# Optimization experiments

Hardware: AMD Instinct MI355X
Metric: run time of the kernel (lower is better)

The kernel has to match this reference:

```python
import jax, jax.numpy as jnp
import numpy as np

CLIP_MIN = 0.0
CLIP_MAX = 1.0
B, T, F, E, CD = 64, 48, 128, 64, 32


def setup_inputs() -> dict:
    key = jax.random.key(0)
    ks = jax.random.split(key, 8)
    return {
        "input_x": jax.random.uniform(ks[0], (B, T, F), dtype=jnp.float32),
        "mask": jax.random.randint(ks[1], (B, T, F), 0, 2, dtype=jnp.int32),
        "embed0": jax.random.normal(ks[2], (F, E), dtype=jnp.float32) * 0.1,
        "embed1": jax.random.normal(ks[3], (F, E), dtype=jnp.float32) * 0.1,
        "embed_missing": jax.random.normal(ks[4], (F, E), dtype=jnp.float32) * 0.1,
        "attention_f_w": jax.random.normal(ks[5], (F, E), dtype=jnp.float32) * 0.1,
        "attention_f_b": jnp.zeros((F,), dtype=jnp.float32),
        "compress_w": jax.random.normal(ks[6], (2 * E, CD), dtype=jnp.float32) * 0.1,
    }


def reference(input_x, mask, embed0, embed1, embed_missing, attention_f_w, attention_f_b, compress_w):
    b, t, f = input_x.shape
    # new_mask: feature observed anywhere in time -> [b, 1, f, 1] (broadcasts over time)
    m = (jnp.sum(mask, axis=-2) != 0).astype(input_x.dtype)[:, None, :, None]
    x = input_x[..., None]  # [b, t, f, 1]
    # interval embedding c: [b, t, f, e]
    c0 = (x - m * CLIP_MIN) * embed0
    c1 = (m * CLIP_MAX - x) * embed1
    c = (c0 + c1) / (CLIP_MAX - CLIP_MIN) + (1.0 - m) * embed_missing
    # pairwise scores: sum_e c_i * c_j * w_i + b_i  (avoids [b,t,f,f,e] materialization)
    scores = jnp.einsum("btie,btje->btij", c * attention_f_w, c) + attention_f_b[:, None]
    scores = jnp.clip(scores, -5.0, 5.0)
    off_diag = 1.0 - jnp.eye(f, dtype=c.dtype)
    masked_exps = jnp.exp(scores) * off_diag
    attn = masked_exps / (jnp.sum(masked_exps, axis=-1, keepdims=True) + 1e-8)  # [b,t,f,f]
    # weighted aggregation: sum_j attn_ij * (c_i * c_j) = c_i * (attn @ c)_i
    agg = c * jnp.einsum("btij,btje->btie", attn, c)
    a = jax.nn.relu(jnp.concatenate([c, agg], axis=-1))  # [b,t,f,2e]
    out = jnp.einsum("btfk,kd->btfd", a, compress_w)
    return out.reshape(b, t, f * compress_w.shape[-1])
```

## Files before the change

### kernel.cpp

```cpp
#include <hip/hip_runtime.h>

#define NB 64
#define NT 48
#define NF 128
#define NE 64
#define NCD 32

#define LOG2E 1.4426950408889634f
#define SCLO -7.213475204444817f
#define SCHI  7.213475204444817f

typedef __attribute__((ext_vector_type(8))) short bf16x8;
typedef __attribute__((ext_vector_type(4))) float f32x4;
typedef __attribute__((ext_vector_type(2))) uint u32x2;

#define WS_MFLAG 0
#define WS_DB    32768
#define WS_E1B   49152
#define WS_EMB   65536
#define WS_WLB   81920
#define WS_WT    98304
#define WS_BL    106496

__device__ __forceinline__ ushort f2bf(float x) {
    union { float f; uint u; } v; v.f = x;
    uint r = v.u + 0x7fffu + ((v.u >> 16) & 1u);
    return (ushort)(r >> 16);
}
__device__ __forceinline__ uint pk_bf16(float lo, float hi) {
    uint r; asm("v_cvt_pk_bf16_f32 %0, %1, %2" : "=v"(r) : "v"(lo), "v"(hi)); return r;
}
__device__ __forceinline__ float bflo(uint u) { union { uint u; float f; } v; v.u = u << 16; return v.f; }
__device__ __forceinline__ float bfhi(uint u) { union { uint u; float f; } v; v.u = u & 0xffff0000u; return v.f; }

#define TRR(dst, addr, IMM) \
    asm volatile("ds_read_b64_tr_b16 %0, %1 offset:" IMM : "=v"(dst) : "v"(addr))

#define PLSWAP(a, b) asm("v_permlane32_swap_b32 %0, %1" : "+v"(a), "+v"(b))

__global__ __launch_bounds__(256) void prep_kernel(
    const int* __restrict__ mask, const float* __restrict__ e0, const float* __restrict__ e1,
    const float* __restrict__ em, const float* __restrict__ aw, const float* __restrict__ ab,
    const float* __restrict__ cw,
    uint* __restrict__ mflag, ushort* __restrict__ db, ushort* __restrict__ e1b,
    ushort* __restrict__ emb, ushort* __restrict__ wlb, ushort* __restrict__ wt,
    float* __restrict__ bl)
{
    const int blk = blockIdx.x, tid = threadIdx.x;
    if (blk < 32) {
        int idx = blk * 256 + tid;
        float e1v = e1[idx];
        e1b[idx] = f2bf(e1v);
        emb[idx] = f2bf(em[idx]);
        db[idx]  = f2bf(e0[idx] - e1v);
        wlb[idx] = f2bf(aw[idx] * LOG2E);
    } else if (blk < 64) {
        int idx = (blk - 32) * 256 + tid;
        int b = idx >> 7, f = idx & 127;
        const int* p = mask + b * (NT * NF) + f;
        int s = 0;
#pragma unroll
        for (int t = 0; t < NT; ++t) s += p[t * NF];
        mflag[idx] = (s != 0) ? 1u : 0u;
    } else if (blk < 80) {
        int idx = (blk - 64) * 256 + tid;
        int k = idx >> 5, d = idx & 31;
        int kd;
        if (k < 64) kd = k;
        else {
            int kk = k - 64;
            kd = 64 + ((kk & 51) | ((kk & 4) << 1) | ((kk & 8) >> 1));
        }
        wt[d * 128 + kd] = f2bf(cw[idx]);
    } else {
        if (tid < NF) bl[tid] = ab[tid] * LOG2E;
    }
}

__global__ __launch_bounds__(512, 4) void fused_kernel(
    const float* __restrict__ input_x, const uint* __restrict__ mflag,
    const ushort* __restrict__ db, const ushort* __restrict__ e1b, const ushort* __restrict__ emb,
    const ushort* __restrict__ wlb, const float* __restrict__ blog,
    const ushort* __restrict__ wt, float* __restrict__ out)
{
    __shared__ ushort sC[2 * 9248];

    const int tid = threadIdx.x;
    const int blk = blockIdx.x;
    const int b   = blk / 24;
    const int bt0 = b * NT + (blk % 24) * 2;
    const int bt1 = bt0 + 1;

    const int wv = tid >> 6, ln = tid & 63;
    const int lr = ln & 15, lg = ln >> 4;
    const int i0 = wv << 4, irow = i0 + lr;

    const float bl = blog[irow];
    const float x0 = input_x[bt0 * NF + irow];
    const float x1 = input_x[bt1 * NF + irow];
    const ushort* Mrow = (mflag[b * NF + irow] ? e1b : emb) + irow * NE;
    const ushort* Drow = db + irow * NE;
    const ushort* Wrow = wlb + irow * NE;

    const int sbase = (lg >> 1) * 2312 + (lr >> 2) * 72 + (lr & 3) * 16 + (lg & 1) * 8;

    ushort* sC0 = sC;
    ushort* sC1 = sC + 9248;

    bf16x8 cwf0[2], cwf1[2];
#pragma unroll
    for (int ks = 0; ks < 2; ++ks) {
        const int eo = ks * 32 + lg * 8;
        uint d4[4], m4[4], w4[4];
        *(uint4*)d4 = *(const uint4*)(Drow + eo);
        *(uint4*)m4 = *(const uint4*)(Mrow + eo);
        *(uint4*)w4 = *(const uint4*)(Wrow + eo);
        uint cb0[4], cb1[4];
        union { uint u[4]; bf16x8 v; } cw0, cw1;
#pragma unroll
        for (int j = 0; j < 4; ++j) {
            float dlo = bflo(d4[j]), dhi = bfhi(d4[j]);
            float mlo = bflo(m4[j]), mhi = bfhi(m4[j]);
            float wlo = bflo(w4[j]), whi = bfhi(w4[j]);
            float c0lo = fmaf(x0, dlo, mlo), c0hi = fmaf(x0, dhi, mhi);
            float c1lo = fmaf(x1, dlo, mlo), c1hi = fmaf(x1, dhi, mhi);
            cb0[j] = pk_bf16(c0lo, c0hi);
            cb1[j] = pk_bf16(c1lo, c1hi);
            cw0.u[j] = pk_bf16(c0lo * wlo, c0hi * whi);
            cw1.u[j] = pk_bf16(c1lo * wlo, c1hi * whi);
        }
        cwf0[ks] = cw0.v; cwf1[ks] = cw1.v;
        *(uint4*)&sC0[sbase + wv * 288 + ks * 4624] = *(uint4*)cb0;
        *(uint4*)&sC1[sbase + wv * 288 + ks * 4624] = *(uint4*)cb1;
    }
    __syncthreads();

    auto run_S = [&](const ushort* base, bf16x8 w0, bf16x8 w1, f32x4* st) {
#pragma unroll
        for (int jt = 0; jt < 8; ++jt) {
            f32x4 a = (f32x4){bl, bl, bl, bl};
            bf16x8 a0 = *(bf16x8*)&base[sbase + jt * 288];
            a = __builtin_amdgcn_mfma_f32_16x16x32_bf16(a0, w0, a, 0, 0, 0);
            bf16x8 a1 = *(bf16x8*)&base[sbase + jt * 288 + 4624];
            a = __builtin_amdgcn_mfma_f32_16x16x32_bf16(a1, w1, a, 0, 0, 0);
            st[jt] = a;
        }
    };
    auto run_SM = [&](f32x4* st, uint* pp) -> float {
        float rs0 = 0.f, rs1 = 0.f, rs2 = 0.f, rs3 = 0.f;
#pragma unroll
        for (int jt = 0; jt < 8; ++jt) {
            f32x4 v = st[jt];
            float e0 = exp2f(__builtin_amdgcn_fmed3f(v[0], SCLO, SCHI));
            float e1 = exp2f(__builtin_amdgcn_fmed3f(v[1], SCLO, SCHI));
            float e2 = exp2f(__builtin_amdgcn_fmed3f(v[2], SCLO, SCHI));
            float e3 = exp2f(__builtin_amdgcn_fmed3f(v[3], SCLO, SCHI));
            if (jt == wv) {
                const bool on = (lg == (lr >> 2));
                e0 = (on && (lr & 3) == 0) ? 0.f : e0;
                e1 = (on && (lr & 3) == 1) ? 0.f : e1;
                e2 = (on && (lr & 3) == 2) ? 0.f : e2;
                e3 = (on && (lr & 3) == 3) ? 0.f : e3;
            }
            rs0 += e0; rs1 += e1; rs2 += e2; rs3 += e3;
            pp[2 * jt]     = pk_bf16(e0, e1);
            pp[2 * jt + 1] = pk_bf16(e2, e3);
        }
        float rs = (rs0 + rs1) + (rs2 + rs3);
        rs += __shfl_xor(rs, 16);
        rs += __shfl_xor(rs, 32);
        return 1.0f / (rs + 1e-8f);
    };
    auto run_AGG = [&](const ushort* base, uint* pp, f32x4* ag) {
#pragma unroll
        for (int et = 0; et < 4; ++et) ag[et] = (f32x4){0.f, 0.f, 0.f, 0.f};
        const uint tb0 = (uint)(uintptr_t)base
                       + 2u * (uint)(72 * (((lg >> 1) << 2) + (lg & 1)) + lr);
#pragma unroll
        for (int ks = 0; ks < 4; ++ks) {
            uint X0 = pp[4 * ks], X1 = pp[4 * ks + 1], X2 = pp[4 * ks + 2], X3 = pp[4 * ks + 3];
            PLSWAP(X0, X2);
            PLSWAP(X1, X3);
            union { uint u[4]; bf16x8 v; } pf;
            pf.u[0] = X0; pf.u[1] = X1; pf.u[2] = X2; pf.u[3] = X3;
            const uint tb = tb0 + 1152u * (uint)ks;
            u32x2 c0a, c0b, c1a, c1b, c2a, c2b, c3a, c3b;
            TRR(c0a, tb, "0");     TRR(c0b, tb, "144");
            TRR(c1a, tb, "4624");  TRR(c1b, tb, "4768");
            TRR(c2a, tb, "9248");  TRR(c2b, tb, "9392");
            TRR(c3a, tb, "13872"); TRR(c3b, tb, "14016");
            asm volatile("s_waitcnt lgkmcnt(0)" ::: "memory");
            __builtin_amdgcn_sched_barrier(0);
            union { u32x2 d[2]; bf16x8 v; } a0, a1, a2, a3;
            a0.d[0] = c0a; a0.d[1] = c0b;
            a1.d[0] = c1a; a1.d[1] = c1b;
            a2.d[0] = c2a; a2.d[1] = c2b;
            a3.d[0] = c3a; a3.d[1] = c3b;
            ag[0] = __builtin_amdgcn_mfma_f32_16x16x32_bf16(a0.v, pf.v, ag[0], 0, 0, 0);
            ag[1] = __builtin_amdgcn_mfma_f32_16x16x32_bf16(a1.v, pf.v, ag[1], 0, 0, 0);
            ag[2] = __builtin_amdgcn_mfma_f32_16x16x32_bf16(a2.v, pf.v, ag[2], 0, 0, 0);
            ag[3] = __builtin_amdgcn_mfma_f32_16x16x32_bf16(a3.v, pf.v, ag[3], 0, 0, 0);
        }
    };
    auto run_EPI = [&](const ushort* base, f32x4* ag, float inv, uint* aa) {
        const int ebase = (wv * 4 + (lr >> 2)) * 72 + (lr & 3) * 16 + lg * 4;
#pragma unroll
        for (int et = 0; et < 4; ++et) {
            u32x2 cb2 = *(u32x2*)&base[ebase + et * 2312];
            float a0f = fmaxf(ag[et][0] * inv * bflo(cb2.x), 0.f);
            float a1f = fmaxf(ag[et][1] * inv * bfhi(cb2.x), 0.f);
            float a2f = fmaxf(ag[et][2] * inv * bflo(cb2.y), 0.f);
            float a3f = fmaxf(ag[et][3] * inv * bfhi(cb2.y), 0.f);
            aa[2 * et]     = pk_bf16(a0f, a1f);
            aa[2 * et + 1] = pk_bf16(a2f, a3f);
        }
    };
    auto run_OUT = [&](const ushort* base, uint* aa, const bf16x8* wf, int bt) {
        f32x4 oc[2];
        oc[0] = (f32x4){0.f, 0.f, 0.f, 0.f};
        oc[1] = (f32x4){0.f, 0.f, 0.f, 0.f};
#pragma unroll
        for (int ks = 0; ks < 4; ++ks) {
            bf16x8 afr;
            if (ks < 2) {
                const uint4 cc = *(uint4*)&base[sbase + wv * 288 + ks * 4624];
                union { uint u[4]; bf16x8 v; } rl;
                asm("v_pk_max_i16 %0, %1, 0" : "=v"(rl.u[0]) : "v"(cc.x));
                asm("v_pk_max_i16 %0, %1, 0" : "=v"(rl.u[1]) : "v"(cc.y));
                asm("v_pk_max_i16 %0, %1, 0" : "=v"(rl.u[2]) : "v"(cc.z));
                asm("v_pk_max_i16 %0, %1, 0" : "=v"(rl.u[3]) : "v"(cc.w));
                afr = rl.v;
            } else {
                const int kk = ks - 2;
                uint Y0 = aa[4 * kk], Y1 = aa[4 * kk + 1], Y2 = aa[4 * kk + 2], Y3 = aa[4 * kk + 3];
                PLSWAP(Y0, Y2);
                PLSWAP(Y1, Y3);
                union { uint u[4]; bf16x8 v; } af;
                af.u[0] = Y0; af.u[1] = Y1; af.u[2] = Y2; af.u[3] = Y3;
                afr = af.v;
            }
            oc[0] = __builtin_amdgcn_mfma_f32_16x16x32_bf16(afr, wf[ks * 2 + 0], oc[0], 0, 0, 0);
            oc[1] = __builtin_amdgcn_mfma_f32_16x16x32_bf16(afr, wf[ks * 2 + 1], oc[1], 0, 0, 0);
        }
        float* op = out + bt * (NF * NCD);
#pragma unroll
        for (int dt = 0; dt < 2; ++dt)
#pragma unroll
            for (int r = 0; r < 4; ++r)
                op[(i0 + lg * 4 + r) * NCD + dt * 16 + lr] = oc[dt][r];
    };

    f32x4 st0[8], st1[8];
    uint pp0[16], pp1[16];
    f32x4 ag0[4], ag1[4];
    uint aa0[8], aa1[8];

    run_S(sC0, cwf0[0], cwf0[1], st0);
    const float inv0 = run_SM(st0, pp0);
    run_S(sC1, cwf1[0], cwf1[1], st1);
    const float inv1 = run_SM(st1, pp1);

    run_AGG(sC0, pp0, ag0);
    run_EPI(sC0, ag0, inv0, aa0);
    run_AGG(sC1, pp1, ag1);

    bf16x8 wf[8];
#pragma unroll
    for (int ks = 0; ks < 4; ++ks)
#pragma unroll
        for (int dt = 0; dt < 2; ++dt)
            wf[ks * 2 + dt] = *(const bf16x8*)(wt + (dt * 16 + lr) * 128 + ks * 32 + lg * 8);

    run_EPI(sC1, ag1, inv1, aa1);
    run_OUT(sC0, aa0, wf, bt0);
    run_OUT(sC1, aa1, wf, bt1);
}

extern "C" void kernel_launch(void* const* d_in, const int* in_sizes, int n_in,
                              void* d_out, int out_size, void* d_ws, size_t ws_size,
                              hipStream_t stream) {
    const float* input_x       = (const float*)d_in[0];
    const int*   mask          = (const int*)d_in[1];
    const float* embed0        = (const float*)d_in[2];
    const float* embed1        = (const float*)d_in[3];
    const float* embed_missing = (const float*)d_in[4];
    const float* attn_w        = (const float*)d_in[5];
    const float* attn_b        = (const float*)d_in[6];
    const float* compress_w    = (const float*)d_in[7];
    float* out = (float*)d_out;

    char* ws = (char*)d_ws;
    uint*   mflag = (uint*)(ws + WS_MFLAG);
    ushort* dbp   = (ushort*)(ws + WS_DB);
    ushort* e1bp  = (ushort*)(ws + WS_E1B);
    ushort* embp  = (ushort*)(ws + WS_EMB);
    ushort* wlbp  = (ushort*)(ws + WS_WLB);
    ushort* wtp   = (ushort*)(ws + WS_WT);
    float*  blp   = (float*)(ws + WS_BL);

    hipLaunchKernelGGL(prep_kernel, dim3(81), dim3(256), 0, stream,
                       mask, embed0, embed1, embed_missing, attn_w, attn_b, compress_w,
                       mflag, dbp, e1bp, embp, wlbp, wtp, blp);
    hipLaunchKernelGGL(fused_kernel, dim3(NB * NT / 2), dim3(512), 0, stream,
                       input_x, mflag, dbp, e1bp, embp, wlbp, blp, wtp, out);
}
```

Before: 43.11 us.

## Halve waves per block, each wave processes two 16-row tiles sharing transposed C loads

The fused kernel now launches 4 waves of 256 threads instead of 8, and each wave handles 32 feature rows as two 16-row groups. In the aggregation step the transposed LDS reads of C are shared between both groups' MFMAs, and the compress stage issues two accumulator sets per wave. This aims to halve redundant LDS traffic per block and increase MFMA work per wave, at the cost of more registers per wave and fewer waves to hide latency.

After: 56.35 us. 1.31x slower.

```diff
diff --git a/kernel.cpp b/kernel.cpp
--- a/kernel.cpp
+++ b/kernel.cpp
@@ -35,7 +35,6 @@
 
 #define TRR(dst, addr, IMM) \
     asm volatile("ds_read_b64_tr_b16 %0, %1 offset:" IMM : "=v"(dst) : "v"(addr))
-
 #define PLSWAP(a, b) asm("v_permlane32_swap_b32 %0, %1" : "+v"(a), "+v"(b))
 
 __global__ __launch_bounds__(256) void prep_kernel(
@@ -77,7 +76,7 @@
     }
 }
 
-__global__ __launch_bounds__(512, 4) void fused_kernel(
+__global__ __launch_bounds__(256, 4) void fused_kernel(
     const float* __restrict__ input_x, const uint* __restrict__ mflag,
     const ushort* __restrict__ db, const ushort* __restrict__ e1b, const ushort* __restrict__ emb,
     const ushort* __restrict__ wlb, const float* __restrict__ blog,
@@ -93,60 +92,67 @@
 
     const int wv = tid >> 6, ln = tid & 63;
     const int lr = ln & 15, lg = ln >> 4;
-    const int i0 = wv << 4, irow = i0 + lr;
-
-    const float bl = blog[irow];
-    const float x0 = input_x[bt0 * NF + irow];
-    const float x1 = input_x[bt1 * NF + irow];
-    const ushort* Mrow = (mflag[b * NF + irow] ? e1b : emb) + irow * NE;
-    const ushort* Drow = db + irow * NE;
-    const ushort* Wrow = wlb + irow * NE;
-
-    const int sbase = (lg >> 1) * 2312 + (lr >> 2) * 72 + (lr & 3) * 16 + (lg & 1) * 8;
+    const int irow0 = wv * 32 + lr;
 
     ushort* sC0 = sC;
     ushort* sC1 = sC + 9248;
 
-    bf16x8 cwf0[2], cwf1[2];
-#pragma unroll
-    for (int ks = 0; ks < 2; ++ks) {
-        const int eo = ks * 32 + lg * 8;
-        uint d4[4], m4[4], w4[4];
-        *(uint4*)d4 = *(const uint4*)(Drow + eo);
-        *(uint4*)m4 = *(const uint4*)(Mrow + eo);
-        *(uint4*)w4 = *(const uint4*)(Wrow + eo);
-        uint cb0[4], cb1[4];
-        union { uint u[4]; bf16x8 v; } cw0, cw1;
-#pragma unroll
-        for (int j = 0; j < 4; ++j) {
-            float dlo = bflo(d4[j]), dhi = bfhi(d4[j]);
-            float mlo = bflo(m4[j]), mhi = bfhi(m4[j]);
-            float wlo = bflo(w4[j]), whi = bfhi(w4[j]);
-            float c0lo = fmaf(x0, dlo, mlo), c0hi = fmaf(x0, dhi, mhi);
-            float c1lo = fmaf(x1, dlo, mlo), c1hi = fmaf(x1, dhi, mhi);
-            cb0[j] = pk_bf16(c0lo, c0hi);
-            cb1[j] = pk_bf16(c1lo, c1hi);
-            cw0.u[j] = pk_bf16(c0lo * wlo, c0hi * whi);
-            cw1.u[j] = pk_bf16(c1lo * wlo, c1hi * whi);
-        }
-        cwf0[ks] = cw0.v; cwf1[ks] = cw1.v;
-        *(uint4*)&sC0[sbase + wv * 288 + ks * 4624] = *(uint4*)cb0;
-        *(uint4*)&sC1[sbase + wv * 288 + ks * 4624] = *(uint4*)cb1;
+    const int abase = (lg >> 1) * 2312 + (lr >> 2) * 72 + (lr & 3) * 16 + (lg & 1) * 8;
+
+    const float bl0 = blog[irow0];
+    const float bl1 = blog[irow0 + 16];
+
+    bf16x8 cwf0[2][2], cwf1[2][2];
+#pragma unroll
+    for (int g = 0; g < 2; ++g) {
+        const int irow = irow0 + g * 16;
+        const float xa = input_x[bt0 * NF + irow];
+        const float xb = input_x[bt1 * NF + irow];
+        const ushort* Mrow = (mflag[b * NF + irow] ? e1b : emb) + irow * NE;
+        const ushort* Drow = db + irow * NE;
+        const ushort* Wrow = wlb + irow * NE;
+#pragma unroll
+        for (int ks = 0; ks < 2; ++ks) {
+            const int eo = ks * 32 + lg * 8;
+            uint d4[4], m4[4], w4[4];
+            *(uint4*)d4 = *(const uint4*)(Drow + eo);
+            *(uint4*)m4 = *(const uint4*)(Mrow + eo);
+            *(uint4*)w4 = *(const uint4*)(Wrow + eo);
+            uint cb0[4], cb1[4];
+            union { uint u[4]; bf16x8 v; } ca, cb;
+#pragma unroll
+            for (int j = 0; j < 4; ++j) {
+                float dlo = bflo(d4[j]), dhi = bfhi(d4[j]);
+                float mlo = bflo(m4[j]), mhi = bfhi(m4[j]);
+                float wlo = bflo(w4[j]), whi = bfhi(w4[j]);
+                float c0lo = fmaf(xa, dlo, mlo), c0hi = fmaf(xa, dhi, mhi);
+                float c1lo = fmaf(xb, dlo, mlo), c1hi = fmaf(xb, dhi, mhi);
+                cb0[j] = pk_bf16(c0lo, c0hi);
+                cb1[j] = pk_bf16(c1lo, c1hi);
+                ca.u[j] = pk_bf16(c0lo * wlo, c0hi * whi);
+                cb.u[j] = pk_bf16(c1lo * wlo, c1hi * whi);
+            }
+            cwf0[g][ks] = ca.v; cwf1[g][ks] = cb.v;
+            const int so = abase + (wv * 2 + g) * 288 + ks * 4624;
+            *(uint4*)&sC0[so] = *(uint4*)cb0;
+            *(uint4*)&sC1[so] = *(uint4*)cb1;
+        }
     }
     __syncthreads();
 
-    auto run_S = [&](const ushort* base, bf16x8 w0, bf16x8 w1, f32x4* st) {
+    auto run_S = [&](const ushort* base, bf16x8 w0, bf16x8 w1, float blv, f32x4* st) {
 #pragma unroll
         for (int jt = 0; jt < 8; ++jt) {
-            f32x4 a = (f32x4){bl, bl, bl, bl};
-            bf16x8 a0 = *(bf16x8*)&base[sbase + jt * 288];
+            f32x4 a = (f32x4){blv, blv, blv, blv};
+            bf16x8 a0 = *(bf16x8*)&base[abase + jt * 288];
             a = __builtin_amdgcn_mfma_f32_16x16x32_bf16(a0, w0, a, 0, 0, 0);
-            bf16x8 a1 = *(bf16x8*)&base[sbase + jt * 288 + 4624];
+            bf16x8 a1 = *(bf16x8*)&base[abase + jt * 288 + 4624];
             a = __builtin_amdgcn_mfma_f32_16x16x32_bf16(a1, w1, a, 0, 0, 0);
             st[jt] = a;
         }
     };
-    auto run_SM = [&](f32x4* st, uint* pp) -> float {
+    auto run_SM = [&](f32x4* st, uint* pp, int g) -> float {
+        const int dt_ = wv * 2 + g;
         float rs0 = 0.f, rs1 = 0.f, rs2 = 0.f, rs3 = 0.f;
 #pragma unroll
         for (int jt = 0; jt < 8; ++jt) {
@@ -155,7 +161,7 @@
             float e1 = exp2f(__builtin_amdgcn_fmed3f(v[1], SCLO, SCHI));
             float e2 = exp2f(__builtin_amdgcn_fmed3f(v[2], SCLO, SCHI));
             float e3 = exp2f(__builtin_amdgcn_fmed3f(v[3], SCLO, SCHI));
-            if (jt == wv) {
+            if (jt == dt_) {
                 const bool on = (lg == (lr >> 2));
                 e0 = (on && (lr & 3) == 0) ? 0.f : e0;
                 e1 = (on && (lr & 3) == 1) ? 0.f : e1;
@@ -171,18 +177,20 @@
         rs += __shfl_xor(rs, 32);
         return 1.0f / (rs + 1e-8f);
     };
-    auto run_AGG = [&](const ushort* base, uint* pp, f32x4* ag) {
-#pragma unroll
-        for (int et = 0; et < 4; ++et) ag[et] = (f32x4){0.f, 0.f, 0.f, 0.f};
+    auto run_AGG = [&](const ushort* base, uint* ppA, uint* ppB, f32x4* agA, f32x4* agB) {
+#pragma unroll
+        for (int et = 0; et < 4; ++et) { agA[et] = (f32x4){0.f,0.f,0.f,0.f}; agB[et] = (f32x4){0.f,0.f,0.f,0.f}; }
         const uint tb0 = (uint)(uintptr_t)base
                        + 2u * (uint)(72 * (((lg >> 1) << 2) + (lg & 1)) + lr);
 #pragma unroll
         for (int ks = 0; ks < 4; ++ks) {
-            uint X0 = pp[4 * ks], X1 = pp[4 * ks + 1], X2 = pp[4 * ks + 2], X3 = pp[4 * ks + 3];
-            PLSWAP(X0, X2);
-            PLSWAP(X1, X3);
-            union { uint u[4]; bf16x8 v; } pf;
-            pf.u[0] = X0; pf.u[1] = X1; pf.u[2] = X2; pf.u[3] = X3;
+            uint XA0 = ppA[4*ks], XA1 = ppA[4*ks+1], XA2 = ppA[4*ks+2], XA3 = ppA[4*ks+3];
+            PLSWAP(XA0, XA2); PLSWAP(XA1, XA3);
+            uint XB0 = ppB[4*ks], XB1 = ppB[4*ks+1], XB2 = ppB[4*ks+2], XB3 = ppB[4*ks+3];
+            PLSWAP(XB0, XB2); PLSWAP(XB1, XB3);
+            union { uint u[4]; bf16x8 v; } pfA, pfB;
+            pfA.u[0] = XA0; pfA.u[1] = XA1; pfA.u[2] = XA2; pfA.u[3] = XA3;
+            pfB.u[0] = XB0; pfB.u[1] = XB1; pfB.u[2] = XB2; pfB.u[3] = XB3;
             const uint tb = tb0 + 1152u * (uint)ks;
             u32x2 c0a, c0b, c1a, c1b, c2a, c2b, c3a, c3b;
             TRR(c0a, tb, "0");     TRR(c0b, tb, "144");
@@ -196,14 +204,18 @@
             a1.d[0] = c1a; a1.d[1] = c1b;
             a2.d[0] = c2a; a2.d[1] = c2b;
             a3.d[0] = c3a; a3.d[1] = c3b;
-            ag[0] = __builtin_amdgcn_mfma_f32_16x16x32_bf16(a0.v, pf.v, ag[0], 0, 0, 0);
-            ag[1] = __builtin_amdgcn_mfma_f32_16x16x32_bf16(a1.v, pf.v, ag[1], 0, 0, 0);
-            ag[2] = __builtin_amdgcn_mfma_f32_16x16x32_bf16(a2.v, pf.v, ag[2], 0, 0, 0);
-            ag[3] = __builtin_amdgcn_mfma_f32_16x16x32_bf16(a3.v, pf.v, ag[3], 0, 0, 0);
-        }
-    };
-    auto run_EPI = [&](const ushort* base, f32x4* ag, float inv, uint* aa) {
-        const int ebase = (wv * 4 + (lr >> 2)) * 72 + (lr & 3) * 16 + lg * 4;
+            agA[0] = __builtin_amdgcn_mfma_f32_16x16x32_bf16(a0.v, pfA.v, agA[0], 0, 0, 0);
+            agB[0] = __builtin_amdgcn_mfma_f32_16x16x32_bf16(a0.v, pfB.v, agB[0], 0, 0, 0);
+            agA[1] = __builtin_amdgcn_mfma_f32_16x16x32_bf16(a1.v, pfA.v, agA[1], 0, 0, 0);
+            agB[1] = __builtin_amdgcn_mfma_f32_16x16x32_bf16(a1.v, pfB.v, agB[1], 0, 0, 0);
+            agA[2] = __builtin_amdgcn_mfma_f32_16x16x32_bf16(a2.v, pfA.v, agA[2], 0, 0, 0);
+            agB[2] = __builtin_amdgcn_mfma_f32_16x16x32_bf16(a2.v, pfB.v, agB[2], 0, 0, 0);
+            agA[3] = __builtin_amdgcn_mfma_f32_16x16x32_bf16(a3.v, pfA.v, agA[3], 0, 0, 0);
+            agB[3] = __builtin_amdgcn_mfma_f32_16x16x32_bf16(a3.v, pfB.v, agB[3], 0, 0, 0);
+        }
+    };
+    auto run_EPI = [&](const ushort* base, f32x4* ag, float inv, uint* aa, int g) {
+        const int ebase = (wv * 8 + g * 4 + (lr >> 2)) * 72 + (lr & 3) * 16 + lg * 4;
 #pragma unroll
         for (int et = 0; et < 4; ++et) {
             u32x2 cb2 = *(u32x2*)&base[ebase + et * 2312];
@@ -215,65 +227,83 @@
             aa[2 * et + 1] = pk_bf16(a2f, a3f);
         }
     };
-    auto run_OUT = [&](const ushort* base, uint* aa, const bf16x8* wf, int bt) {
-        f32x4 oc[2];
-        oc[0] = (f32x4){0.f, 0.f, 0.f, 0.f};
-        oc[1] = (f32x4){0.f, 0.f, 0.f, 0.f};
+    auto run_OUT = [&](const ushort* base, uint* aaA, uint* aaB, const bf16x8* wf, int bt) {
+        f32x4 ocA[2], ocB[2];
+        ocA[0] = (f32x4){0.f,0.f,0.f,0.f}; ocA[1] = (f32x4){0.f,0.f,0.f,0.f};
+        ocB[0] = (f32x4){0.f,0.f,0.f,0.f}; ocB[1] = (f32x4){0.f,0.f,0.f,0.f};
 #pragma unroll
         for (int ks = 0; ks < 4; ++ks) {
-            bf16x8 afr;
+            bf16x8 afrA, afrB;
             if (ks < 2) {
-                const uint4 cc = *(uint4*)&base[sbase + wv * 288 + ks * 4624];
-                union { uint u[4]; bf16x8 v; } rl;
-                asm("v_pk_max_i16 %0, %1, 0" : "=v"(rl.u[0]) : "v"(cc.x));
-                asm("v_pk_max_i16 %0, %1, 0" : "=v"(rl.u[1]) : "v"(cc.y));
-                asm("v_pk_max_i16 %0, %1, 0" : "=v"(rl.u[2]) : "v"(cc.z));
-                asm("v_pk_max_i16 %0, %1, 0" : "=v"(rl.u[3]) : "v"(cc.w));
-                afr = rl.v;
+                const uint4 ccA = *(uint4*)&base[abase + (wv * 2 + 0) * 288 + ks * 4624];
+                const uint4 ccB = *(uint4*)&base[abase + (wv * 2 + 1) * 288 + ks * 4624];
+                union { uint u[4]; bf16x8 v; } rA, rB;
+                asm("v_pk_max_i16 %0, %1, 0" : "=v"(rA.u[0]) : "v"(ccA.x));
+                asm("v_pk_max_i16 %0, %1, 0" : "=v"(rA.u[1]) : "v"(ccA.y));
+                asm("v_pk_max_i16 %0, %1, 0" : "=v"(rA.u[2]) : "v"(ccA.z));
+                asm("v_pk_max_i16 %0, %1, 0" : "=v"(rA.u[3]) : "v"(ccA.w));
+                asm("v_pk_max_i16 %0, %1, 0" : "=v"(rB.u[0]) : "v"(ccB.x));
+                asm("v_pk_max_i16 %0, %1, 0" : "=v"(rB.u[1]) : "v"(ccB.y));
+                asm("v_pk_max_i16 %0, %1, 0" : "=v"(rB.u[2]) : "v"(ccB.z));
+                asm("v_pk_max_i16 %0, %1, 0" : "=v"(rB.u[3]) : "v"(ccB.w));
+                afrA = rA.v; afrB = rB.v;
             } else {
                 const int kk = ks - 2;
-                uint Y0 = aa[4 * kk], Y1 = aa[4 * kk + 1], Y2 = aa[4 * kk + 2], Y3 = aa[4 * kk + 3];
-                PLSWAP(Y0, Y2);
-                PLSWAP(Y1, Y3);
-                union { uint u[4]; bf16x8 v; } af;
-                af.u[0] = Y0; af.u[1] = Y1; af.u[2] = Y2; af.u[3] = Y3;
-                afr = af.v;
+                uint YA0 = aaA[4*kk], YA1 = aaA[4*kk+1], YA2 = aaA[4*kk+2], YA3 = aaA[4*kk+3];
+                PLSWAP(YA0, YA2); PLSWAP(YA1, YA3);
+                uint YB0 = aaB[4*kk], YB1 = aaB[4*kk+1], YB2 = aaB[4*kk+2], YB3 = aaB[4*kk+3];
+                PLSWAP(YB0, YB2); PLSWAP(YB1, YB3);
+                union { uint u[4]; bf16x8 v; } fA, fB;
+                fA.u[0] = YA0; fA.u[1] = YA1; fA.u[2] = YA2; fA.u[3] = YA3;
+                fB.u[0] = YB0; fB.u[1] = YB1; fB.u[2] = YB2; fB.u[3] = YB3;
+                afrA = fA.v; afrB = fB.v;
             }
-            oc[0] = __builtin_amdgcn_mfma_f32_16x16x32_bf16(afr, wf[ks * 2 + 0], oc[0], 0, 0, 0);
-            oc[1] = __builtin_amdgcn_mfma_f32_16x16x32_bf16(afr, wf[ks * 2 + 1], oc[1], 0, 0, 0);
+            ocA[0] = __builtin_amdgcn_mfma_f32_16x16x32_bf16(afrA, wf[ks*2+0], ocA[0], 0, 0, 0);
+            ocA[1] = __builtin_amdgcn_mfma_f32_16x16x32_bf16(afrA, wf[ks*2+1], ocA[1], 0, 0, 0);
+            ocB[0] = __builtin_amdgcn_mfma_f32_16x16x32_bf16(afrB, wf[ks*2+0], ocB[0], 0, 0, 0);
+            ocB[1] = __builtin_amdgcn_mfma_f32_16x16x32_bf16(afrB, wf[ks*2+1], ocB[1], 0, 0, 0);
         }
         float* op = out + bt * (NF * NCD);
 #pragma unroll
-        for (int dt = 0; dt < 2; ++dt)
-#pragma unroll
-            for (int r = 0; r < 4; ++r)
-                op[(i0 + lg * 4 + r) * NCD + dt * 16 + lr] = oc[dt][r];
-    };
-
-    f32x4 st0[8], st1[8];
+        for (int dt2 = 0; dt2 < 2; ++dt2)
+#pragma unroll
+            for (int r = 0; r < 4; ++r) {
+                op[(wv * 32 + lg * 4 + r) * NCD + dt2 * 16 + lr]      = ocA[dt2][r];
+                op[(wv * 32 + 16 + lg * 4 + r) * NCD + dt2 * 16 + lr] = ocB[dt2][r];
+            }
+    };
+
+    f32x4 st[8];
     uint pp0[16], pp1[16];
-    f32x4 ag0[4], ag1[4];
-    uint aa0[8], aa1[8];
-
-    run_S(sC0, cwf0[0], cwf0[1], st0);
-    const float inv0 = run_SM(st0, pp0);
-    run_S(sC1, cwf1[0], cwf1[1], st1);
-    const float inv1 = run_SM(st1, pp1);
-
-    run_AGG(sC0, pp0, ag0);
-    run_EPI(sC0, ag0, inv0, aa0);
-    run_AGG(sC1, pp1, ag1);
+    f32x4 agA[4], agB[4];
+    uint aa00[8], aa01[8], aa10[8], aa11[8];
+
+    run_S(sC0, cwf0[0][0], cwf0[0][1], bl0, st);
+    const float i00 = run_SM(st, pp0, 0);
+    run_S(sC0, cwf0[1][0], cwf0[1][1], bl1, st);
+    const float i01 = run_SM(st, pp1, 1);
+    run_AGG(sC0, pp0, pp1, agA, agB);
+    run_EPI(sC0, agA, i00, aa00, 0);
+    run_EPI(sC0, agB, i01, aa01, 1);
+
+    run_S(sC1, cwf1[0][0], cwf1[0][1], bl0, st);
+    const float i10 = run_SM(st, pp0, 0);
+    run_S(sC1, cwf1[1][0], cwf1[1][1], bl1, st);
+    const float i11 = run_SM(st, pp1, 1);
+    run_AGG(sC1, pp0, pp1, agA, agB);
 
     bf16x8 wf[8];
 #pragma unroll
     for (int ks = 0; ks < 4; ++ks)
 #pragma unroll
-        for (int dt = 0; dt < 2; ++dt)
-            wf[ks * 2 + dt] = *(const bf16x8*)(wt + (dt * 16 + lr) * 128 + ks * 32 + lg * 8);
-
-    run_EPI(sC1, ag1, inv1, aa1);
-    run_OUT(sC0, aa0, wf, bt0);
-    run_OUT(sC1, aa1, wf, bt1);
+        for (int dt2 = 0; dt2 < 2; ++dt2)
+            wf[ks * 2 + dt2] = *(const bf16x8*)(wt + (dt2 * 16 + lr) * 128 + ks * 32 + lg * 8);
+
+    run_EPI(sC1, agA, i10, aa10, 0);
+    run_EPI(sC1, agB, i11, aa11, 1);
+
+    run_OUT(sC0, aa00, aa01, wf, bt0);
+    run_OUT(sC1, aa10, aa11, wf, bt1);
 }
 
 extern "C" void kernel_launch(void* const* d_in, const int* in_sizes, int n_in,
@@ -301,6 +331,6 @@
     hipLaunchKernelGGL(prep_kernel, dim3(81), dim3(256), 0, stream,
                        mask, embed0, embed1, embed_missing, attn_w, attn_b, compress_w,
                        mflag, dbp, e1bp, embp, wlbp, wtp, blp);
-    hipLaunchKernelGGL(fused_kernel, dim3(NB * NT / 2), dim3(512), 0, stream,
+    hipLaunchKernelGGL(fused_kernel, dim3(NB * NT / 2), dim3(256), 0, stream,
                        input_x, mflag, dbp, e1bp, embp, wlbp, blp, wtp, out);
 }
```
